# Kernel optimization log

Hardware: AMD Instinct MI355X
Metric: run time of the kernel (lower is better)

Reference implementation:

```python
import jax, jax.numpy as jnp
import numpy as np

CTX = 2048   # context_window
D   = 256    # emb_dim
B   = 16     # batch
C   = 2048   # sequence length (<= CTX)


def make_rotary_matrix(ctx, d):
    """Dense per-position rotation matrix, as in the tinyllama get_rotary_matrix:
    theta_i = 10000 ** (-2*(i-1)/d), 2x2 rotation blocks on the diagonal."""
    pos = np.arange(ctx, dtype=np.float64)[:, None]            # [ctx, 1]
    i = np.arange(d // 2, dtype=np.float64)                    # [d/2]
    theta = 10000.0 ** (-2.0 * (i - 1.0) / d)                  # note (i-1), matches source
    ang = pos * theta                                          # [ctx, d/2]
    c, s = np.cos(ang), np.sin(ang)
    R = np.zeros((ctx, d, d), dtype=np.float32)
    k = np.arange(d // 2)
    R[:, 2 * k, 2 * k] = c
    R[:, 2 * k, 2 * k + 1] = -s
    R[:, 2 * k + 1, 2 * k] = s
    R[:, 2 * k + 1, 2 * k + 1] = c
    return jnp.asarray(R)


def setup_inputs() -> dict:
    key = jax.random.key(0)
    ks = jax.random.split(key, 4)
    scale = 1.0 / np.sqrt(D)
    x = jax.random.normal(ks[0], (B, C, D), dtype=jnp.float32)
    Wq = jax.random.normal(ks[1], (D, D), dtype=jnp.float32) * scale
    Wk = jax.random.normal(ks[2], (D, D), dtype=jnp.float32) * scale
    Wv = jax.random.normal(ks[3], (D, D), dtype=jnp.float32) * scale
    bq = jnp.zeros((D,), dtype=jnp.float32)
    bk = jnp.zeros((D,), dtype=jnp.float32)
    bv = jnp.zeros((D,), dtype=jnp.float32)
    R = make_rotary_matrix(CTX, D)
    return {"x": x, "Wq": Wq, "bq": bq, "Wk": Wk, "bk": bk, "Wv": Wv, "bv": bv, "R": R}


def reference(x, Wq, bq, Wk, bk, Wv, bv, R):
    Bz, Cz, d = x.shape
    # QKV projections (torch Linear: y = x @ W.T + b)
    q = x @ Wq.T + bq
    k = x @ Wk.T + bk
    v = x @ Wv.T + bv
    # Dense rotary: q_rot[b,c,:] = R[c] @ q[b,c,:]  (original: bmm(q^T, R[:C]^T)^T)
    Rc = R[:Cz]                                        # [C, D, D]
    q_rot = jnp.einsum('bcd,ced->bce', q, Rc)          # [B, C, D]
    k_rot = jnp.einsum('bcd,ced->bce', k, Rc)          # [B, C, D]
    # Causal SDPA (dropout_p=0.2 in source -> disabled here, eval-mode determinism)
    scale = 1.0 / jnp.sqrt(jnp.asarray(d, dtype=x.dtype))
    scores = jnp.einsum('bqd,bkd->bqk', q_rot, k_rot) * scale   # [B, C, C]
    causal = jnp.tril(jnp.ones((Cz, Cz), dtype=bool))
    scores = jnp.where(causal, scores, jnp.asarray(-jnp.inf, dtype=scores.dtype))
    attn = jax.nn.softmax(scores, axis=-1)
    out = jnp.einsum('bqk,bkd->bqd', attn, v)                   # [B, C, D]
    return out
```

## Files before the change

### kernel.cpp

```cpp
#include <hip/hip_runtime.h>
#include <stdint.h>

#define BB 16
#define CC 2048
#define DD 256
#define MM (BB*CC)

typedef __attribute__((ext_vector_type(4))) float f32x4;
typedef __attribute__((ext_vector_type(8))) short bf16x8;
typedef __attribute__((ext_vector_type(4))) short s16x4;

static __device__ __forceinline__ short f2bf(float f) {
  union { float f; uint32_t u; } v; v.f = f;
  uint32_t u = v.u;
  return (short)((u + 0x7FFFu + ((u >> 16) & 1u)) >> 16);
}

#define GLDS16(gp, lp) __builtin_amdgcn_global_load_lds(                      \
    (const __attribute__((address_space(1))) void*)(gp),                      \
    (__attribute__((address_space(3))) void*)(lp), 16, 0, 0)

#define DPP_ROR_F(x, n) __uint_as_float(__builtin_amdgcn_update_dpp(          \
    0, (int)__float_as_uint(x), 0x120 + (n), 0xF, 0xF, false))

__global__ __launch_bounds__(256) void k_trig(float2* __restrict__ cs) {
  int id = blockIdx.x * 256 + threadIdx.x;
  int k = id & 127, pg = id >> 7;
  double th = pow(10000.0, (1.0 - (double)k) * (1.0 / 128.0));
  const double TWO_PI = 6.283185307179586476925287;
  const double INV_2PI = 1.0 / TWO_PI;
  #pragma unroll
  for (int i = 0; i < 16; ++i) {
    int pos = pg * 16 + i;
    double ang = (double)pos * th;
    double red = ang - floor(ang * INV_2PI) * TWO_PI;
    float fr = (float)red;
    cs[(size_t)pos * 128 + k] = make_float2(__cosf(fr), __sinf(fr));
  }
}

__global__ __launch_bounds__(256) void k_wconv(
    const float* __restrict__ Wq, const float* __restrict__ Wk,
    const float* __restrict__ Wv, short* __restrict__ wb) {
  int gid = blockIdx.x * 256 + threadIdx.x;
  int mat = gid >> 14;
  int rem = gid & 16383;
  int kc = rem >> 11;
  int o  = (rem & 2047) * 8;
  int e  = o >> 6;
  int c4 = ((o & 63) ^ (((e >> 1) & 3) << 4)) >> 3;
  const float* W = (mat == 0) ? Wq : (mat == 1) ? Wk : Wv;
  f32x4 wv = *(const f32x4*)(W + (size_t)e * DD + kc * 32 + c4 * 4);
  s16x4 b4;
  b4[0] = f2bf(wv[0]); b4[1] = f2bf(wv[1]); b4[2] = f2bf(wv[2]); b4[3] = f2bf(wv[3]);
  *(s16x4*)((char*)wb + (size_t)gid * 8) = b4;
}

__global__ __launch_bounds__(256, 2) void k_qkv(
    const float* __restrict__ x, const short* __restrict__ wb,
    const float* __restrict__ bq, const float* __restrict__ bk,
    const float* __restrict__ bv, const float2* __restrict__ cs,
    short* __restrict__ q_rot, short* __restrict__ k_rot,
    short* __restrict__ v_t)
{
  __shared__ char SM[32768 + 49152];
  short* xs = (short*)SM;
  char* wsh = SM + 32768;
  const int t = threadIdx.x;
  const int lane = t & 63, w = t >> 6;
  const int g = lane >> 4, li = lane & 15;
  const int m0 = blockIdx.x * 64;

  #pragma unroll
  for (int i = 0; i < 16; ++i) {
    int chunk = i * 256 + t;
    int row = chunk >> 6, c4 = chunk & 63;
    f32x4 xv = *(const f32x4*)(x + (size_t)(m0 + row) * DD + c4 * 4);
    s16x4 b4;
    b4[0] = f2bf(xv[0]); b4[1] = f2bf(xv[1]); b4[2] = f2bf(xv[2]); b4[3] = f2bf(xv[3]);
    *(s16x4*)((char*)xs + row * 512 + ((c4 * 8) ^ ((row & 7) << 4))) = b4;
  }
  __syncthreads();

  f32x4 zero4 = {0.f, 0.f, 0.f, 0.f};
  f32x4 accQ[16], accK[16], accV[16];
  #pragma unroll
  for (int nt = 0; nt < 16; ++nt) { accQ[nt] = zero4; accK[nt] = zero4; accV[nt] = zero4; }

  for (int kc = 0; kc < 8; ++kc) {
    #pragma unroll
    for (int i = 0; i < 12; ++i) {
      int cc = i * 4 + w;
      const char* src = (const char*)wb + (size_t)(cc >> 4) * 131072 +
                        kc * 16384 + (cc & 15) * 1024 + lane * 16;
      GLDS16(src, wsh + cc * 1024);
    }
    asm volatile("s_waitcnt vmcnt(0)" ::: "memory");
    __builtin_amdgcn_sched_barrier(0);
    __builtin_amdgcn_s_barrier();

    const int arow = w * 16 + li;
    bf16x8 a = *(const bf16x8*)((char*)xs + arow * 512 +
                                (((kc * 64) + g * 16) ^ ((arow & 7) << 4)));
    #pragma unroll
    for (int nt = 0; nt < 16; ++nt) {
      int e = nt * 16 + li;
      int off = e * 64 + ((g * 16) ^ (((e >> 1) & 3) << 4));
      bf16x8 fq = *(const bf16x8*)(wsh + off);
      bf16x8 fk = *(const bf16x8*)(wsh + 16384 + off);
      bf16x8 fv = *(const bf16x8*)(wsh + 32768 + off);
      accQ[nt] = __builtin_amdgcn_mfma_f32_16x16x32_bf16(a, fq, accQ[nt], 0, 0, 0);
      accK[nt] = __builtin_amdgcn_mfma_f32_16x16x32_bf16(a, fk, accK[nt], 0, 0, 0);
      accV[nt] = __builtin_amdgcn_mfma_f32_16x16x32_bf16(a, fv, accV[nt], 0, 0, 0);
    }
    __builtin_amdgcn_s_barrier();
  }

  __syncthreads();
  {
    char* Tq = SM;
    char* Tk = SM + 33792;
    #pragma unroll
    for (int nt = 0; nt < 16; ++nt) {
      int e = nt * 16 + li;
      float bQ = bq[e], bK = bk[e];
      #pragma unroll
      for (int r = 0; r < 4; ++r) {
        int cloc = w * 16 + g * 4 + r;
        int m = m0 + cloc;
        float2 csv = cs[(size_t)(m & (CC - 1)) * 128 + (e >> 1)];
        float vq = accQ[nt][r] + bQ;
        float oq = __shfl_xor(vq, 1);
        vq = csv.x * vq + ((e & 1) ? csv.y * oq : -csv.y * oq);
        *(short*)(Tq + cloc * 528 + e * 2) = f2bf(vq * 0.0625f);
        float vk = accK[nt][r] + bK;
        float ok = __shfl_xor(vk, 1);
        vk = csv.x * vk + ((e & 1) ? csv.y * ok : -csv.y * ok);
        *(short*)(Tk + cloc * 528 + e * 2) = f2bf(vk);
      }
    }
    __syncthreads();
    #pragma unroll
    for (int it = 0; it < 8; ++it) {
      int chunk = it * 256 + t;
      int c = chunk >> 5, e32 = chunk & 31;
      int4 vq4 = *(const int4*)(Tq + c * 528 + e32 * 16);
      int4 vk4 = *(const int4*)(Tk + c * 528 + e32 * 16);
      *(int4*)(q_rot + (size_t)(m0 + c) * DD + e32 * 8) = vq4;
      *(int4*)(k_rot + (size_t)(m0 + c) * DD + e32 * 8) = vk4;
    }
  }
  __syncthreads();
  #pragma unroll
  for (int nt = 0; nt < 16; ++nt) {
    int e = nt * 16 + li;
    float bias = bv[e];
    #pragma unroll
    for (int r = 0; r < 4; ++r) {
      int cloc = w * 16 + g * 4 + r;
      *(short*)(SM + e * 144 + cloc * 2) = f2bf(accV[nt][r] + bias);
    }
  }
  __syncthreads();
  {
    const int bb = m0 >> 11, c0 = m0 & (CC - 1);
    #pragma unroll
    for (int it = 0; it < 8; ++it) {
      int chunk = it * 256 + t;
      int e = chunk >> 3, c8 = chunk & 7;
      int4 vv = *(const int4*)(SM + e * 144 + c8 * 16);
      *(int4*)(v_t + ((size_t)(bb * DD + e)) * CC + c0 + c8 * 8) = vv;
    }
  }
}

__global__ __launch_bounds__(512, 2) void k_attn(
    const short* __restrict__ q_rot, const short* __restrict__ k_rot,
    const short* __restrict__ v_t, float* __restrict__ out)
{
  __shared__ char SM[143360];
  const int t = threadIdx.x;
  const int lane = t & 63, w = t >> 6;
  const int wg = w & 3, gq = w >> 2;
  const int g = lane >> 4, li = lane & 15;

  const int p = blockIdx.x;
  const int b = p & 15;
  const int j = p >> 4;

  const short* kbase = k_rot + (size_t)b * CC * DD;
  const short* vbase = v_t  + (size_t)b * DD * CC;

  float* U  = (float*)(SM + 65536);
  float* ML = (float*)(SM + 142848);
  char* Pb = SM + 132608 + w * 1280;

  f32x4 zero4 = {0.f, 0.f, 0.f, 0.f};

  for (int tt = 0; tt < 2; ++tt) {
    const int qt = tt ? (31 - j) : j;
    const int q0 = qt * 64;
    const int NTg = qt + 1;
    const int kvoff = gq * 32 * NTg;

    const short* qb = q_rot + ((size_t)b * CC + q0 + wg * 16 + li) * DD;
    bf16x8 qf[8];
    #pragma unroll
    for (int dc = 0; dc < 8; ++dc)
      qf[dc] = *(const bf16x8*)(qb + dc * 32 + g * 8);

    f32x4 O[16];
    #pragma unroll
    for (int i = 0; i < 16; ++i) O[i] = zero4;
    float mrow[4], lrow[4];
    #pragma unroll
    for (int r = 0; r < 4; ++r) { mrow[r] = -__builtin_inff(); lrow[r] = 0.f; }

    auto STAGE = [&](int buf, int kt) {
      const int k0s = kvoff + kt * 32;
      char* dst = SM + (size_t)(gq * 2 + buf) * 32768;
      #pragma unroll
      for (int i = 0; i < 4; ++i) {
        int c = i * 4 + wg;
        int row = 2 * c + (lane >> 5);
        int cb = ((lane & 31) * 16) ^ ((row & 7) << 4);
        const char* src = (const char*)(kbase + (size_t)(k0s + row) * DD) + cb;
        GLDS16(src, dst + c * 1024);
      }
      #pragma unroll
      for (int i = 0; i < 4; ++i) {
        int c = i * 4 + wg;
        int d = 16 * c + (lane >> 2);
        int sb = (((lane & 3) ^ ((lane >> 3) & 3)) * 16);
        const char* src = (const char*)(vbase + (size_t)d * CC + k0s) + sb;
        GLDS16(src, dst + 16384 + c * 1024);
      }
    };

    int cur = 0;
    STAGE(0, 0);
    for (int kt = 0; kt < NTg; ++kt) {
      const int k0 = kvoff + kt * 32;
      asm volatile("s_waitcnt vmcnt(0)" ::: "memory");
      __builtin_amdgcn_sched_barrier(0);
      __builtin_amdgcn_s_barrier();
      if (kt + 1 < NTg) STAGE(cur ^ 1, kt + 1);

      const char* Kb = SM + (size_t)(gq * 2 + cur) * 32768;
      const char* Vb = Kb + 16384;

      f32x4 S[2];
      S[0] = zero4; S[1] = zero4;
      __builtin_amdgcn_s_setprio(1);
      #pragma unroll
      for (int dc = 0; dc < 8; ++dc) {
        #pragma unroll
        for (int nt = 0; nt < 2; ++nt) {
          int krow = nt * 16 + li;
          bf16x8 kf = *(const bf16x8*)(Kb + krow * 512 +
                                       (((dc * 64) + g * 16) ^ ((krow & 7) << 4)));
          S[nt] = __builtin_amdgcn_mfma_f32_16x16x32_bf16(qf[dc], kf, S[nt], 0, 0, 0);
        }
      }
      __builtin_amdgcn_s_setprio(0);

      if (k0 + 31 > q0) {
        #pragma unroll
        for (int nt = 0; nt < 2; ++nt)
          #pragma unroll
          for (int r = 0; r < 4; ++r)
            if ((k0 + nt * 16 + li) > (q0 + wg * 16 + g * 4 + r))
              S[nt][r] = -1.0e30f;
      }

      float mxr[4];
      #pragma unroll
      for (int r = 0; r < 4; ++r) {
        float mx = fmaxf(S[0][r], S[1][r]);
        mx = fmaxf(mx, DPP_ROR_F(mx, 8));
        mx = fmaxf(mx, DPP_ROR_F(mx, 4));
        mx = fmaxf(mx, DPP_ROR_F(mx, 2));
        mx = fmaxf(mx, DPP_ROR_F(mx, 1));
        mxr[r] = mx;
      }
      int need = 0;
      #pragma unroll
      for (int r = 0; r < 4; ++r) need |= (mxr[r] > mrow[r] + 8.f) ? 1 : 0;
      if (__any(need)) {
        #pragma unroll
        for (int r = 0; r < 4; ++r) {
          float mnew = fmaxf(mrow[r], mxr[r]);
          float al = __expf(mrow[r] - mnew);
          mrow[r] = mnew;
          lrow[r] *= al;
          #pragma unroll
          for (int dt2 = 0; dt2 < 16; ++dt2) O[dt2][r] *= al;
        }
      }
      #pragma unroll
      for (int r = 0; r < 4; ++r) {
        float rsum = 0.f;
        #pragma unroll
        for (int nt = 0; nt < 2; ++nt) {
          float pv = __expf(S[nt][r] - mrow[r]);
          S[nt][r] = pv;
          rsum += pv;
        }
        rsum += DPP_ROR_F(rsum, 8);
        rsum += DPP_ROR_F(rsum, 4);
        rsum += DPP_ROR_F(rsum, 2);
        rsum += DPP_ROR_F(rsum, 1);
        lrow[r] += rsum;
      }

      #pragma unroll
      for (int nt = 0; nt < 2; ++nt)
        #pragma unroll
        for (int r = 0; r < 4; ++r)
          *(short*)(Pb + (g * 4 + r) * 80 + (nt * 16 + li) * 2) = f2bf(S[nt][r]);

      bf16x8 pf = *(const bf16x8*)(Pb + li * 80 + g * 16);

      __builtin_amdgcn_s_setprio(1);
      #pragma unroll
      for (int dt2 = 0; dt2 < 16; ++dt2) {
        bf16x8 vf = *(const bf16x8*)(Vb + (dt2 * 16 + li) * 64 +
                                     ((g * 16) ^ (((li >> 1) & 3) << 4)));
        O[dt2] = __builtin_amdgcn_mfma_f32_16x16x32_bf16(pf, vf, O[dt2], 0, 0, 0);
      }
      __builtin_amdgcn_s_setprio(0);
      cur ^= 1;
    }

    __syncthreads();
    if (gq == 1) {
      #pragma unroll
      for (int r = 0; r < 4; ++r) {
        int row = wg * 16 + g * 4 + r;
        if (li == 0) { ML[row * 2] = mrow[r]; ML[row * 2 + 1] = lrow[r]; }
        #pragma unroll
        for (int dt2 = 0; dt2 < 16; ++dt2)
          U[row * 260 + dt2 * 16 + li] = O[dt2][r];
      }
    }
    __syncthreads();
    if (gq == 0) {
      float eA[4], eB[4], invl[4];
      #pragma unroll
      for (int r = 0; r < 4; ++r) {
        int row = wg * 16 + g * 4 + r;
        float mB = ML[row * 2], lB = ML[row * 2 + 1];
        float m = fmaxf(mrow[r], mB);
        eA[r] = __expf(mrow[r] - m);
        eB[r] = __expf(mB - m);
        invl[r] = 1.f / (lrow[r] * eA[r] + lB * eB[r]);
      }
      #pragma unroll
      for (int dt2 = 0; dt2 < 16; ++dt2)
        #pragma unroll
        for (int r = 0; r < 4; ++r) {
          int row = wg * 16 + g * 4 + r;
          float uB = U[row * 260 + dt2 * 16 + li];
          out[((size_t)b * CC + q0 + row) * DD + dt2 * 16 + li] =
              (O[dt2][r] * eA[r] + uB * eB[r]) * invl[r];
        }
    }
    __syncthreads();
  }
}

extern "C" void kernel_launch(void* const* d_in, const int* in_sizes, int n_in,
                              void* d_out, int out_size, void* d_ws, size_t ws_size,
                              hipStream_t stream) {
  const float* x  = (const float*)d_in[0];
  const float* Wq = (const float*)d_in[1];
  const float* bq = (const float*)d_in[2];
  const float* Wk = (const float*)d_in[3];
  const float* bk = (const float*)d_in[4];
  const float* Wv = (const float*)d_in[5];
  const float* bv = (const float*)d_in[6];
  float* out = (float*)d_out;
  (void)in_sizes; (void)n_in; (void)out_size; (void)ws_size;

  char* ws = (char*)d_ws;
  float2* cs   = (float2*)ws;
  short* q_rot = (short*)(ws + (2u << 20));
  short* k_rot = q_rot + (size_t)MM * DD;
  short* v_tr  = k_rot + (size_t)MM * DD;
  short* wb    = v_tr + (size_t)MM * DD;

  k_trig <<<  64, 256, 0, stream>>>(cs);
  k_wconv<<< 192, 256, 0, stream>>>(Wq, Wk, Wv, wb);
  k_qkv  <<< 512, 256, 0, stream>>>(x, wb, bq, bk, bv, cs, q_rot, k_rot, v_tr);
  k_attn <<< 256, 512, 0, stream>>>(q_rot, k_rot, v_tr, out);
}
```

Baseline: 121.7 us.

## Merge prep kernels, enlarge QKV tile, double-buffer weight staging

```diff
diff --git a/kernel.cpp b/kernel.cpp
--- a/kernel.cpp
+++ b/kernel.cpp
@@ -23,63 +23,78 @@
 #define DPP_ROR_F(x, n) __uint_as_float(__builtin_amdgcn_update_dpp(          \
     0, (int)__float_as_uint(x), 0x120 + (n), 0xF, 0xF, false))
 
-__global__ __launch_bounds__(256) void k_trig(float2* __restrict__ cs) {
-  int id = blockIdx.x * 256 + threadIdx.x;
-  int k = id & 127, pg = id >> 7;
-  double th = pow(10000.0, (1.0 - (double)k) * (1.0 / 128.0));
-  const double TWO_PI = 6.283185307179586476925287;
-  const double INV_2PI = 1.0 / TWO_PI;
-  #pragma unroll
-  for (int i = 0; i < 16; ++i) {
-    int pos = pg * 16 + i;
-    double ang = (double)pos * th;
-    double red = ang - floor(ang * INV_2PI) * TWO_PI;
-    float fr = (float)red;
-    cs[(size_t)pos * 128 + k] = make_float2(__cosf(fr), __sinf(fr));
-  }
-}
-
-__global__ __launch_bounds__(256) void k_wconv(
+__global__ __launch_bounds__(256) void k_prep(
     const float* __restrict__ Wq, const float* __restrict__ Wk,
-    const float* __restrict__ Wv, short* __restrict__ wb) {
-  int gid = blockIdx.x * 256 + threadIdx.x;
-  int mat = gid >> 14;
-  int rem = gid & 16383;
-  int kc = rem >> 11;
-  int o  = (rem & 2047) * 8;
-  int e  = o >> 6;
-  int c4 = ((o & 63) ^ (((e >> 1) & 3) << 4)) >> 3;
-  const float* W = (mat == 0) ? Wq : (mat == 1) ? Wk : Wv;
-  f32x4 wv = *(const f32x4*)(W + (size_t)e * DD + kc * 32 + c4 * 4);
-  s16x4 b4;
-  b4[0] = f2bf(wv[0]); b4[1] = f2bf(wv[1]); b4[2] = f2bf(wv[2]); b4[3] = f2bf(wv[3]);
-  *(s16x4*)((char*)wb + (size_t)gid * 8) = b4;
-}
-
-__global__ __launch_bounds__(256, 2) void k_qkv(
+    const float* __restrict__ Wv, short* __restrict__ wb,
+    float2* __restrict__ cs) {
+  const int bid = blockIdx.x;
+  if (bid < 64) {
+    int id = bid * 256 + threadIdx.x;
+    int k = id & 127, pg = id >> 7;
+    double th = pow(10000.0, (1.0 - (double)k) * (1.0 / 128.0));
+    const double TWO_PI = 6.283185307179586476925287;
+    const double INV_2PI = 1.0 / TWO_PI;
+    #pragma unroll
+    for (int i = 0; i < 16; ++i) {
+      int pos = pg * 16 + i;
+      double ang = (double)pos * th;
+      double red = ang - floor(ang * INV_2PI) * TWO_PI;
+      float fr = (float)red;
+      cs[(size_t)pos * 128 + k] = make_float2(__cosf(fr), __sinf(fr));
+    }
+  } else {
+    int gid = (bid - 64) * 256 + threadIdx.x;
+    int s = gid / 3072;
+    int og = gid - s * 3072;
+    int mat = og >> 10;
+    int o = (og & 1023) * 8;
+    int e_local = o >> 6;
+    int e = (s & 1) * 128 + e_local;
+    int kc = s >> 1;
+    int c4 = ((o & 63) ^ (((e >> 1) & 3) << 4)) >> 3;
+    const float* W = (mat == 0) ? Wq : (mat == 1) ? Wk : Wv;
+    f32x4 wv = *(const f32x4*)(W + (size_t)e * DD + kc * 32 + c4 * 4);
+    s16x4 b4;
+    b4[0] = f2bf(wv[0]); b4[1] = f2bf(wv[1]); b4[2] = f2bf(wv[2]); b4[3] = f2bf(wv[3]);
+    *(s16x4*)((char*)wb + (size_t)gid * 8) = b4;
+  }
+}
+
+__global__ __launch_bounds__(512, 2) void k_qkv(
     const float* __restrict__ x, const short* __restrict__ wb,
     const float* __restrict__ bq, const float* __restrict__ bk,
     const float* __restrict__ bv, const float2* __restrict__ cs,
     short* __restrict__ q_rot, short* __restrict__ k_rot,
     short* __restrict__ v_t)
 {
-  __shared__ char SM[32768 + 49152];
+  __shared__ char SM[114688];
   short* xs = (short*)SM;
-  char* wsh = SM + 32768;
+  char* wsh = SM + 65536;
   const int t = threadIdx.x;
   const int lane = t & 63, w = t >> 6;
   const int g = lane >> 4, li = lane & 15;
-  const int m0 = blockIdx.x * 64;
+  const int m0 = blockIdx.x * 128;
 
   #pragma unroll
   for (int i = 0; i < 16; ++i) {
-    int chunk = i * 256 + t;
+    int chunk = i * 512 + t;
     int row = chunk >> 6, c4 = chunk & 63;
     f32x4 xv = *(const f32x4*)(x + (size_t)(m0 + row) * DD + c4 * 4);
     s16x4 b4;
     b4[0] = f2bf(xv[0]); b4[1] = f2bf(xv[1]); b4[2] = f2bf(xv[2]); b4[3] = f2bf(xv[3]);
     *(s16x4*)((char*)xs + row * 512 + ((c4 * 8) ^ ((row & 7) << 4))) = b4;
   }
+
+  auto STAGE = [&](int buf, int s) {
+    #pragma unroll
+    for (int i = 0; i < 3; ++i) {
+      int cc = i * 8 + w;
+      const char* src = (const char*)wb + s * 24576 + cc * 1024 + lane * 16;
+      GLDS16(src, wsh + buf * 24576 + cc * 1024);
+    }
+  };
+
+  STAGE(0, 0);
   __syncthreads();
 
   f32x4 zero4 = {0.f, 0.f, 0.f, 0.f};
@@ -87,67 +102,52 @@
   #pragma unroll
   for (int nt = 0; nt < 16; ++nt) { accQ[nt] = zero4; accK[nt] = zero4; accV[nt] = zero4; }
 
+  #pragma unroll
   for (int kc = 0; kc < 8; ++kc) {
     #pragma unroll
-    for (int i = 0; i < 12; ++i) {
-      int cc = i * 4 + w;
-      const char* src = (const char*)wb + (size_t)(cc >> 4) * 131072 +
-                        kc * 16384 + (cc & 15) * 1024 + lane * 16;
-      GLDS16(src, wsh + cc * 1024);
-    }
-    asm volatile("s_waitcnt vmcnt(0)" ::: "memory");
-    __builtin_amdgcn_sched_barrier(0);
-    __builtin_amdgcn_s_barrier();
-
-    const int arow = w * 16 + li;
-    bf16x8 a = *(const bf16x8*)((char*)xs + arow * 512 +
-                                (((kc * 64) + g * 16) ^ ((arow & 7) << 4)));
-    #pragma unroll
-    for (int nt = 0; nt < 16; ++nt) {
-      int e = nt * 16 + li;
-      int off = e * 64 + ((g * 16) ^ (((e >> 1) & 3) << 4));
-      bf16x8 fq = *(const bf16x8*)(wsh + off);
-      bf16x8 fk = *(const bf16x8*)(wsh + 16384 + off);
-      bf16x8 fv = *(const bf16x8*)(wsh + 32768 + off);
-      accQ[nt] = __builtin_amdgcn_mfma_f32_16x16x32_bf16(a, fq, accQ[nt], 0, 0, 0);
-      accK[nt] = __builtin_amdgcn_mfma_f32_16x16x32_bf16(a, fk, accK[nt], 0, 0, 0);
-      accV[nt] = __builtin_amdgcn_mfma_f32_16x16x32_bf16(a, fv, accV[nt], 0, 0, 0);
-    }
-    __builtin_amdgcn_s_barrier();
-  }
-
-  __syncthreads();
-  {
-    char* Tq = SM;
-    char* Tk = SM + 33792;
-    #pragma unroll
-    for (int nt = 0; nt < 16; ++nt) {
-      int e = nt * 16 + li;
-      float bQ = bq[e], bK = bk[e];
-      #pragma unroll
-      for (int r = 0; r < 4; ++r) {
-        int cloc = w * 16 + g * 4 + r;
-        int m = m0 + cloc;
-        float2 csv = cs[(size_t)(m & (CC - 1)) * 128 + (e >> 1)];
-        float vq = accQ[nt][r] + bQ;
-        float oq = __shfl_xor(vq, 1);
-        vq = csv.x * vq + ((e & 1) ? csv.y * oq : -csv.y * oq);
-        *(short*)(Tq + cloc * 528 + e * 2) = f2bf(vq * 0.0625f);
-        float vk = accK[nt][r] + bK;
-        float ok = __shfl_xor(vk, 1);
-        vk = csv.x * vk + ((e & 1) ? csv.y * ok : -csv.y * ok);
-        *(short*)(Tk + cloc * 528 + e * 2) = f2bf(vk);
-      }
-    }
-    __syncthreads();
-    #pragma unroll
-    for (int it = 0; it < 8; ++it) {
-      int chunk = it * 256 + t;
-      int c = chunk >> 5, e32 = chunk & 31;
-      int4 vq4 = *(const int4*)(Tq + c * 528 + e32 * 16);
-      int4 vk4 = *(const int4*)(Tk + c * 528 + e32 * 16);
-      *(int4*)(q_rot + (size_t)(m0 + c) * DD + e32 * 8) = vq4;
-      *(int4*)(k_rot + (size_t)(m0 + c) * DD + e32 * 8) = vk4;
+    for (int eh = 0; eh < 2; ++eh) {
+      const int s = kc * 2 + eh;
+      asm volatile("s_waitcnt vmcnt(0)" ::: "memory");
+      __builtin_amdgcn_sched_barrier(0);
+      __builtin_amdgcn_s_barrier();
+      if (s + 1 < 16) STAGE((s + 1) & 1, s + 1);
+
+      const int arow = w * 16 + li;
+      bf16x8 a = *(const bf16x8*)((char*)xs + arow * 512 +
+                                  (((kc * 64) + g * 16) ^ ((arow & 7) << 4)));
+      const char* Wb = wsh + (s & 1) * 24576;
+      #pragma unroll
+      for (int ntl = 0; ntl < 8; ++ntl) {
+        const int nt = eh * 8 + ntl;
+        int e_local = ntl * 16 + li;
+        int e = eh * 128 + e_local;
+        int off = e_local * 64 + ((g * 16) ^ (((e >> 1) & 3) << 4));
+        bf16x8 fq = *(const bf16x8*)(Wb + off);
+        bf16x8 fk = *(const bf16x8*)(Wb + 8192 + off);
+        bf16x8 fv = *(const bf16x8*)(Wb + 16384 + off);
+        accQ[nt] = __builtin_amdgcn_mfma_f32_16x16x32_bf16(a, fq, accQ[nt], 0, 0, 0);
+        accK[nt] = __builtin_amdgcn_mfma_f32_16x16x32_bf16(a, fk, accK[nt], 0, 0, 0);
+        accV[nt] = __builtin_amdgcn_mfma_f32_16x16x32_bf16(a, fv, accV[nt], 0, 0, 0);
+      }
+    }
+  }
+
+  #pragma unroll
+  for (int nt = 0; nt < 16; ++nt) {
+    int e = nt * 16 + li;
+    float bQ = bq[e], bK = bk[e];
+    #pragma unroll
+    for (int r = 0; r < 4; ++r) {
+      int m = m0 + w * 16 + g * 4 + r;
+      float2 csv = cs[(size_t)(m & (CC - 1)) * 128 + (e >> 1)];
+      float vq = accQ[nt][r] + bQ;
+      float oq = __shfl_xor(vq, 1);
+      vq = csv.x * vq + ((e & 1) ? csv.y * oq : -csv.y * oq);
+      q_rot[(size_t)m * DD + e] = f2bf(vq * 0.0625f);
+      float vk = accK[nt][r] + bK;
+      float ok = __shfl_xor(vk, 1);
+      vk = csv.x * vk + ((e & 1) ? csv.y * ok : -csv.y * ok);
+      k_rot[(size_t)m * DD + e] = f2bf(vk);
     }
   }
   __syncthreads();
@@ -158,7 +158,7 @@
     #pragma unroll
     for (int r = 0; r < 4; ++r) {
       int cloc = w * 16 + g * 4 + r;
-      *(short*)(SM + e * 144 + cloc * 2) = f2bf(accV[nt][r] + bias);
+      *(short*)(SM + e * 272 + cloc * 2) = f2bf(accV[nt][r] + bias);
     }
   }
   __syncthreads();
@@ -166,9 +166,9 @@
     const int bb = m0 >> 11, c0 = m0 & (CC - 1);
     #pragma unroll
     for (int it = 0; it < 8; ++it) {
-      int chunk = it * 256 + t;
-      int e = chunk >> 3, c8 = chunk & 7;
-      int4 vv = *(const int4*)(SM + e * 144 + c8 * 16);
+      int chunk = it * 512 + t;
+      int e = chunk >> 4, c8 = chunk & 15;
+      int4 vv = *(const int4*)(SM + e * 272 + c8 * 16);
       *(int4*)(v_t + ((size_t)(bb * DD + e)) * CC + c0 + c8 * 8) = vv;
     }
   }
@@ -389,8 +389,7 @@
   short* v_tr  = k_rot + (size_t)MM * DD;
   short* wb    = v_tr + (size_t)MM * DD;
 
-  k_trig <<<  64, 256, 0, stream>>>(cs);
-  k_wconv<<< 192, 256, 0, stream>>>(Wq, Wk, Wv, wb);
-  k_qkv  <<< 512, 256, 0, stream>>>(x, wb, bq, bk, bv, cs, q_rot, k_rot, v_tr);
+  k_prep <<< 256, 256, 0, stream>>>(Wq, Wk, Wv, wb, cs);
+  k_qkv  <<< 256, 512, 0, stream>>>(x, wb, bq, bk, bv, cs, q_rot, k_rot, v_tr);
   k_attn <<< 256, 512, 0, stream>>>(q_rot, k_rot, v_tr, out);
 }
```

New measurement: 145.0 us. 19.2% more time.
